# Performance work log

Measured on AMD Instinct MI355X. Metric: run time of the kernel, lower is better.

Reference implementation:

```python
import jax, jax.numpy as jnp
import numpy as np

NUM_HEADS = 12

def _get_rel_pos(q_size, k_size, rel_pos):
    # rel_pos already has shape (2*max(q,k)-1, head_dim) -> no resize needed
    q_coords = jnp.arange(q_size)[:, None] * max(k_size / q_size, 1.0)
    k_coords = jnp.arange(k_size)[None, :] * max(q_size / k_size, 1.0)
    rel = (q_coords - k_coords + (k_size - 1) * max(q_size / k_size, 1.0)).astype(jnp.int32)
    return rel_pos[rel.reshape(-1)].reshape(q_size, k_size, -1)  # (q, k, head_dim)


def setup_inputs() -> dict:
    key = jax.random.key(0)
    ks = jax.random.split(key, 7)
    B, H, W, C = 1, 64, 64, 768
    head_dim = C // NUM_HEADS
    return {
        "x": jax.random.normal(ks[0], (B, H, W, C), jnp.float32),
        "qkv_w": jax.random.normal(ks[1], (C, 3 * C), jnp.float32) * 0.02,
        "qkv_b": jax.random.normal(ks[2], (3 * C,), jnp.float32) * 0.02,
        "rel_pos_h": jax.random.normal(ks[3], (2 * H - 1, head_dim), jnp.float32) * 0.02,
        "rel_pos_w": jax.random.normal(ks[4], (2 * W - 1, head_dim), jnp.float32) * 0.02,
        "proj_w": jax.random.normal(ks[5], (C, C), jnp.float32) * 0.02,
        "proj_b": jax.random.normal(ks[6], (C,), jnp.float32) * 0.02,
    }


def reference(x, qkv_w, qkv_b, rel_pos_h, rel_pos_w, proj_w, proj_b):
    B, H, W, C = x.shape
    nh = NUM_HEADS
    hd = C // nh
    scale = hd ** (-0.5)
    S = H * W

    qkv = x @ qkv_w + qkv_b                              # (B,H,W,3C)
    qkv = qkv.reshape(B, S, 3, nh, hd).transpose(2, 0, 3, 1, 4).reshape(3, B * nh, S, hd)
    q, k, v = qkv[0], qkv[1], qkv[2]                     # (B*nh, S, hd)

    attn = jnp.einsum('bqd,bkd->bqk', q * scale, k)      # (B*nh, S, S)

    rh = _get_rel_pos(H, H, rel_pos_h)                   # (H,H,hd)
    rw = _get_rel_pos(W, W, rel_pos_w)                   # (W,W,hd)
    r_q = q.reshape(B * nh, H, W, hd)
    rel_h = jnp.einsum('bhwc,hkc->bhwk', r_q, rh)        # (B*nh,H,W,H)
    rel_w = jnp.einsum('bhwc,wkc->bhwk', r_q, rw)        # (B*nh,H,W,W)
    attn = (attn.reshape(B * nh, H, W, H, W)
            + rel_h[:, :, :, :, None]
            + rel_w[:, :, :, None, :]).reshape(B * nh, S, S)

    attn = jax.nn.softmax(attn, axis=-1)
    out = jnp.einsum('bqk,bkd->bqd', attn, v)            # (B*nh, S, hd)
    out = out.reshape(B, nh, H, W, hd).transpose(0, 2, 3, 1, 4).reshape(B, H, W, C)
    return out @ proj_w + proj_b
```

## Files before the change

### kernel.cpp

```cpp
#include <hip/hip_runtime.h>
#include <hip/hip_bf16.h>

#define S_TOK 4096
#define CDIM  768
#define N3C   2304
#define NH    12
#define HD    64

#define LOG2E 1.44269504f

typedef __attribute__((ext_vector_type(8))) short short8;
typedef __attribute__((ext_vector_type(4))) short short4v;
typedef __attribute__((ext_vector_type(4))) float float4v;
typedef __attribute__((ext_vector_type(4))) unsigned uint4v;

__device__ __forceinline__ float b2f(short s) {
    return __uint_as_float(((unsigned)(unsigned short)s) << 16);
}
__device__ __forceinline__ short f2b(float f) {
    unsigned u = __float_as_uint(f);
    unsigned r = (u + 0x7FFFu + ((u >> 16) & 1u)) >> 16;
    return (short)r;
}

#if __has_builtin(__builtin_amdgcn_exp2f)
#define EXP2F __builtin_amdgcn_exp2f
#else
#define EXP2F exp2f
#endif

__device__ __forceinline__ unsigned pack_trunc(float a, float b) {
    return __builtin_amdgcn_perm(__float_as_uint(b), __float_as_uint(a), 0x07060302u);
}

__device__ __forceinline__ short8 u4_to_s8(unsigned a, unsigned b, unsigned c, unsigned d) {
    union { uint4v u; short8 s; } t;
    t.u = (uint4v){a, b, c, d};
    return t.s;
}

__device__ __forceinline__ void load_lds16(const void* g, void* l) {
    __builtin_amdgcn_global_load_lds(
        (const __attribute__((address_space(1))) unsigned int*)g,
        (__attribute__((address_space(3))) unsigned int*)l, 16, 0, 0);
}

__global__ __launch_bounds__(256) void cast_bf16_kernel(
    const float* __restrict__ in, short* __restrict__ out, int n4)
{
    int i = blockIdx.x * 256 + threadIdx.x;
    if (i >= n4) return;
    float4 v = ((const float4*)in)[i];
    short4v o4 = { f2b(v.x), f2b(v.y), f2b(v.z), f2b(v.w) };
    *(short4v*)&out[(size_t)i * 4] = o4;
}

__global__ __launch_bounds__(256) void transpose_cast_kernel(
    const float* __restrict__ in, short* __restrict__ out, int R, int C)
{
    __shared__ float t[64][65];
    const int tid = threadIdx.x;
    const int c0 = blockIdx.x * 64, r0 = blockIdx.y * 64;
    const int li = tid >> 6;
    const int lj = tid & 63;
#pragma unroll
    for (int p = 0; p < 16; ++p) {
        int i = p * 4 + li;
        t[i][lj] = in[(size_t)(r0 + i) * C + c0 + lj];
    }
    __syncthreads();
#pragma unroll
    for (int p = 0; p < 16; ++p) {
        int i = p * 4 + li;
        out[(size_t)(c0 + i) * R + r0 + lj] = f2b(t[lj][i]);
    }
}

#define GEMM_CORE(A_, Bt_)                                                     \
    __shared__ __align__(16) short smem[2][128][64];                           \
    auto a_s = smem[0];                                                        \
    auto b_s = smem[1];                                                        \
    const int tid  = threadIdx.x;                                              \
    const int m0 = blockIdx.y * 128;                                           \
    const int n0 = blockIdx.x * 128;                                           \
    const int lane = tid & 63, w = tid >> 6;                                   \
    const int l15 = lane & 15, quad = lane >> 4;                               \
    const int wr = w >> 1, wc = w & 1;                                         \
    const int roff0 = (quad ^ (l15 & 7)) << 4;                                 \
    const int roff1 = roff0 ^ 64;                                              \
    const int srow0 = w * 8 + (lane >> 3);                                     \
    const int sslot = (lane & 7) ^ ((lane >> 3) & 7);                          \
    const short* ga = A_ + (size_t)(m0 + srow0) * 768 + sslot * 8;             \
    const short* gb = Bt_ + (size_t)(n0 + srow0) * 768 + sslot * 8;            \
    short* la = &a_s[w * 8][0];                                                \
    short* lb = &b_s[w * 8][0];                                                \
    float4v acc[4][4];                                                         \
    _Pragma("unroll")                                                          \
    for (int i = 0; i < 4; ++i)                                                \
        _Pragma("unroll")                                                      \
        for (int j = 0; j < 4; ++j) acc[i][j] = (float4v){0.f,0.f,0.f,0.f};    \
    for (int k0 = 0; k0 < 768; k0 += 64) {                                     \
        __syncthreads();                                                       \
        _Pragma("unroll")                                                      \
        for (int i = 0; i < 4; ++i) {                                          \
            load_lds16(ga + (size_t)i * (32 * 768) + k0, la + i * 32 * 64);    \
            load_lds16(gb + (size_t)i * (32 * 768) + k0, lb + i * 32 * 64);    \
        }                                                                      \
        __syncthreads();                                                       \
        _Pragma("unroll")                                                      \
        for (int kk = 0; kk < 64; kk += 32) {                                  \
            const int roff = kk ? roff1 : roff0;                               \
            short8 af[4], bfr[4];                                              \
            _Pragma("unroll")                                                  \
            for (int i = 0; i < 4; ++i)                                        \
                af[i] = *(const short8*)((const char*)&a_s[wr*64 + i*16 + l15][0] + roff); \
            _Pragma("unroll")                                                  \
            for (int j = 0; j < 4; ++j)                                        \
                bfr[j] = *(const short8*)((const char*)&b_s[wc*64 + j*16 + l15][0] + roff); \
            _Pragma("unroll")                                                  \
            for (int i = 0; i < 4; ++i)                                        \
                _Pragma("unroll")                                              \
                for (int j = 0; j < 4; ++j)                                    \
                    acc[i][j] = __builtin_amdgcn_mfma_f32_16x16x32_bf16(       \
                        af[i], bfr[j], acc[i][j], 0, 0, 0);                    \
        }                                                                      \
    }

__global__ __launch_bounds__(256) void gemm_qkv_mfma(
    const short* __restrict__ A, const short* __restrict__ Bt,
    const float* __restrict__ bias,
    short* __restrict__ Qb, short* __restrict__ Kb, short* __restrict__ Vt)
{
    GEMM_CORE(A, Bt)

    const int sec = n0 / CDIM;
    float bj[4];
#pragma unroll
    for (int j = 0; j < 4; ++j) bj[j] = bias[n0 + wc*64 + j*16 + l15];

    if (sec < 2) {
        short* base = (sec == 0) ? Qb : Kb;
        short (*tile)[68] = (short(*)[68])&smem[0][0][0];
#pragma unroll
        for (int h = 0; h < 2; ++h) {
            __syncthreads();
            if (wc == h) {
#pragma unroll
                for (int i = 0; i < 4; ++i)
#pragma unroll
                    for (int j = 0; j < 4; ++j)
#pragma unroll
                        for (int r = 0; r < 4; ++r)
                            tile[wr*64 + i*16 + quad*4 + r][j*16 + l15] =
                                f2b(acc[i][j][r] + bj[j]);
            }
            __syncthreads();
            const int nn = (n0 % CDIM) + h * 64;
            const int head = nn >> 6;
            short* dst = base + ((size_t)head * S_TOK + m0) * HD;
#pragma unroll
            for (int it = 0; it < 4; ++it) {
                const int row = it * 32 + (tid >> 3), c = (tid & 7) * 8;
                *(short8*)&dst[(size_t)row * HD + c] = *(const short8*)&tile[row][c];
            }
        }
    } else {
        short (*tv)[130] = (short(*)[130])&smem[0][0][0];
#pragma unroll
        for (int h = 0; h < 2; ++h) {
            __syncthreads();
            if (wc == h) {
#pragma unroll
                for (int i = 0; i < 4; ++i)
#pragma unroll
                    for (int j = 0; j < 4; ++j) {
                        short4v v4;
#pragma unroll
                        for (int r = 0; r < 4; ++r) v4[r] = f2b(acc[i][j][r] + bj[j]);
                        *(short4v*)&tv[j*16 + l15][wr*64 + i*16 + quad*4] = v4;
                    }
            }
            __syncthreads();
            const int nn = (n0 % CDIM) + h * 64;
            const int head = nn >> 6;
            short* dst = Vt + (size_t)head * HD * S_TOK + m0;
#pragma unroll
            for (int it = 0; it < 4; ++it) {
                const int nr = it * 16 + (tid >> 4), sc = (tid & 15) * 8;
                *(short8*)&dst[(size_t)nr * S_TOK + sc] = *(const short8*)&tv[nr][sc];
            }
        }
    }
}

__global__ __launch_bounds__(256) void gemm_proj_mfma(
    const short* __restrict__ A, const short* __restrict__ Bt,
    const float* __restrict__ bias, float* __restrict__ out)
{
    GEMM_CORE(A, Bt)

    float bj[4];
#pragma unroll
    for (int j = 0; j < 4; ++j) bj[j] = bias[n0 + wc*64 + j*16 + l15];

    float* tf = (float*)&smem[0][0][0];
#pragma unroll
    for (int h = 0; h < 2; ++h) {
        __syncthreads();
        if (wr == h) {
#pragma unroll
            for (int i = 0; i < 4; ++i)
#pragma unroll
                for (int j = 0; j < 4; ++j) {
                    const int cc = wc*16 + j*4 + (l15 >> 2);
                    const int ci = l15 & 3;
#pragma unroll
                    for (int r = 0; r < 4; ++r) {
                        const int row = i*16 + quad*4 + r;
                        const int pc = cc ^ ((row & 7) << 2);
                        tf[row * 128 + pc * 4 + ci] = acc[i][j][r] + bj[j];
                    }
                }
        }
        __syncthreads();
        float* dst = out + (size_t)(m0 + h * 64) * CDIM + n0;
#pragma unroll
        for (int it = 0; it < 8; ++it) {
            const int row = it * 8 + (tid >> 5);
            const int gc = tid & 31;
            const int pc = gc ^ ((row & 7) << 2);
            float4 v = *(const float4*)&tf[row * 128 + pc * 4];
            *(float4*)&dst[(size_t)row * CDIM + gc * 4] = v;
        }
    }
}

__global__ __launch_bounds__(256) void rel_mfma_kernel(
    const short* __restrict__ Qb, const float* __restrict__ rph,
    const float* __restrict__ rpw, short* __restrict__ RelhT,
    short* __restrict__ Relw)
{
    __shared__ __align__(16) short q_s [64][72];
    __shared__ __align__(16) short rh_s[64][72];
    __shared__ __align__(16) short rw_s[128][72];

    const int tid  = threadIdx.x;
    const int y    = blockIdx.x;
    const int head = blockIdx.y;
    const int s0   = y * 64;
    const int w = tid >> 6, lane = tid & 63;
    const int l15 = lane & 15, quad = lane >> 4;
    const int srow = tid >> 2;
    const int scol = (tid & 3) << 4;

    {
        const uint4* g = (const uint4*)(Qb + ((size_t)head * S_TOK + s0 + srow) * HD + scol);
        *(uint4*)&q_s[srow][scol]     = g[0];
        *(uint4*)&q_s[srow][scol + 8] = g[1];
    }
    {
        const float* g = rph + (size_t)(y + srow) * HD + scol;
        short tmp[16];
#pragma unroll
        for (int i = 0; i < 16; i += 4) {
            float4 v = *(const float4*)(g + i);
            tmp[i] = f2b(v.x); tmp[i+1] = f2b(v.y); tmp[i+2] = f2b(v.z); tmp[i+3] = f2b(v.w);
        }
        *(short8*)&rh_s[srow][scol]     = *(short8*)&tmp[0];
        *(short8*)&rh_s[srow][scol + 8] = *(short8*)&tmp[8];
    }
#pragma unroll
    for (int half = 0; half < 2; ++half) {
        const int row = srow + half * 64;
        const int rr  = row > 126 ? 126 : row;
        const float* g = rpw + (size_t)rr * HD + scol;
        short tmp[16];
#pragma unroll
        for (int i = 0; i < 16; i += 4) {
            float4 v = *(const float4*)(g + i);
            tmp[i] = f2b(v.x); tmp[i+1] = f2b(v.y); tmp[i+2] = f2b(v.z); tmp[i+3] = f2b(v.w);
        }
        *(short8*)&rw_s[row][scol]     = *(short8*)&tmp[0];
        *(short8*)&rw_s[row][scol + 8] = *(short8*)&tmp[8];
    }
    __syncthreads();

    const short8 qa0 = *(const short8*)&q_s[w * 16 + l15][quad * 8];
    const short8 qa1 = *(const short8*)&q_s[w * 16 + l15][32 + quad * 8];

#pragma unroll
    for (int ct = 0; ct < 4; ++ct) {
        const int jj = ct * 16 + l15;
        short8 b0 = *(const short8*)&rh_s[jj][quad * 8];
        short8 b1 = *(const short8*)&rh_s[jj][32 + quad * 8];
        float4v z = (float4v){0.f, 0.f, 0.f, 0.f};
        z = __builtin_amdgcn_mfma_f32_16x16x32_bf16(qa0, b0, z, 0, 0, 0);
        z = __builtin_amdgcn_mfma_f32_16x16x32_bf16(qa1, b1, z, 0, 0, 0);
        const int ky = 63 - jj;
        short4v o4;
#pragma unroll
        for (int r = 0; r < 4; ++r) o4[r] = f2b(z[r] * LOG2E);
        *(short4v*)&RelhT[((size_t)head * HD + ky) * S_TOK + s0 + w * 16 + quad * 4] = o4;
    }

#pragma unroll
    for (int ct = 0; ct < 8; ++ct) {
        const int j = ct * 16 + l15;
        short8 b0 = *(const short8*)&rw_s[j][quad * 8];
        short8 b1 = *(const short8*)&rw_s[j][32 + quad * 8];
        float4v z = (float4v){0.f, 0.f, 0.f, 0.f};
        z = __builtin_amdgcn_mfma_f32_16x16x32_bf16(qa0, b0, z, 0, 0, 0);
        z = __builtin_amdgcn_mfma_f32_16x16x32_bf16(qa1, b1, z, 0, 0, 0);
#pragma unroll
        for (int r = 0; r < 4; ++r) {
            const int q  = w * 16 + quad * 4 + r;
            const int kx = q + 63 - j;
            if (kx >= 0 && kx < 64)
                Relw[((size_t)head * S_TOK + s0 + q) * HD + kx] = f2b(z[r] * LOG2E);
        }
    }
}

__global__ __launch_bounds__(256, 3) void flash_kernel(
    const short* __restrict__ Qb, const short* __restrict__ Kb,
    const short* __restrict__ Vt, const short* __restrict__ RelhT,
    const short* __restrict__ Relw, short* __restrict__ attn_b)
{
    __shared__ __align__(16) short lds_s[24576];

    const int tid  = threadIdx.x;
    const int bid  = blockIdx.x;
    const int logi = (bid & 7) * 96 + (bid >> 3);
    const int head = logi >> 6;
    const int s0   = (logi & 63) << 6;
    const int w    = tid >> 6, lane = tid & 63;
    const int l15  = lane & 15, quad = lane >> 4;
    const int ph   = w >> 1;
    const int qh   = w & 1;

    const float C1 = 0.125f * LOG2E;

    const int lj = lane >> 3;
    const int sl = (lane & 7) ^ lj;
    const int kf0 = (lj & 3) + ((lj & 4) << 1) + qh * 32;

    const short* pKs = Kb + (size_t)head * S_TOK * HD
                     + (size_t)(ph * 32 * 64 + kf0) * HD + sl * 8;
    const short* pVs = Vt + ((size_t)head * HD + qh * 32 + lj) * S_TOK
                     + ph * 32 * 64 + sl * 8;

    short* lk0 = &lds_s[(ph * 2 + 0) << 12] + qh * 32 * 64;
    short* lk1 = &lds_s[(ph * 2 + 1) << 12] + qh * 32 * 64;
    short* lv  = &lds_s[16384 + (ph << 12)] + qh * 32 * 64;
    const short* krd0 = &lds_s[(ph * 2 + 0) << 12];
    const short* krd1 = &lds_s[(ph * 2 + 1) << 12];
    const short* vrd  = &lds_s[16384 + (ph << 12)];

    const int roff0 = (quad ^ (l15 & 7)) << 4;
    const int roff1 = roff0 ^ 64;

    short8 qb[2][2];
#pragma unroll
    for (int qt = 0; qt < 2; ++qt) {
        const short* qrow = Qb + ((size_t)head * S_TOK + s0 + qh * 32 + qt * 16 + l15) * HD;
        qb[qt][0] = *(const short8*)(qrow + quad * 8);
        qb[qt][1] = *(const short8*)(qrow + 32 + quad * 8);
    }

    float rwv[2][4][4];
#pragma unroll
    for (int qt = 0; qt < 2; ++qt) {
        const short* rwrow = Relw + ((size_t)head * S_TOK + s0 + qh * 32 + qt * 16 + l15) * HD;
#pragma unroll
        for (int kt = 0; kt < 4; ++kt) {
            const int base = ((kt & 1) << 2) | ((kt >> 1) << 5);
            short4v v = *(const short4v*)(rwrow + base + quad * 8);
#pragma unroll
            for (int r = 0; r < 4; ++r) rwv[qt][kt][r] = b2f(v[r]);
        }
    }

    const short* rhbase = RelhT + (size_t)head * HD * S_TOK + s0 + qh * 32 + l15;
    float rhc0 = b2f(rhbase[(size_t)(ph * 32) * S_TOK]);
    float rhc1 = b2f(rhbase[(size_t)(ph * 32) * S_TOK + 16]);

    short8 aones;
#pragma unroll
    for (int j = 0; j < 8; ++j) aones[j] = (short)0x3F80;

    float4v od[2][4];
#pragma unroll
    for (int qt = 0; qt < 2; ++qt)
#pragma unroll
        for (int dt = 0; dt < 4; ++dt) od[qt][dt] = (float4v){0.f, 0.f, 0.f, 0.f};
    float4v dq0 = (float4v){0.f, 0.f, 0.f, 0.f};
    float4v dq1 = (float4v){0.f, 0.f, 0.f, 0.f};

    load_lds16(pKs,        lk0);
    load_lds16(pKs + 1024, lk0 + 8  * 64);
    load_lds16(pKs + 256,  lk0 + 16 * 64);
    load_lds16(pKs + 1280, lk0 + 24 * 64);
    __syncthreads();

    for (int t = 0; t < 32; ++t) {
        const int cur = t & 1;
        const short* krd = cur ? krd1 : krd0;
        short* lkn = cur ? lk0 : lk1;

        load_lds16(pVs,               lv);
        load_lds16(pVs + 8  * S_TOK,  lv + 8  * 64);
        load_lds16(pVs + 16 * S_TOK,  lv + 16 * 64);
        load_lds16(pVs + 24 * S_TOK,  lv + 24 * 64);
        if (t < 31) {
            const short* pk = pKs + 4096;
            load_lds16(pk,        lkn);
            load_lds16(pk + 1024, lkn + 8  * 64);
            load_lds16(pk + 256,  lkn + 16 * 64);
            load_lds16(pk + 1280, lkn + 24 * 64);
        }
        pKs += 4096;
        pVs += 64;

        short rhn0, rhn1;
        if (t < 31) {
            rhn0 = rhbase[(size_t)(ph * 32 + t + 1) * S_TOK];
            rhn1 = rhbase[(size_t)(ph * 32 + t + 1) * S_TOK + 16];
        }

        unsigned pkk[2][8];
#pragma unroll
        for (int kt = 0; kt < 4; ++kt) {
            const char* krp = (const char*)(krd + (kt * 16 + l15) * 64);
            const short8 ka0 = *(const short8*)(krp + roff0);
            const short8 ka1 = *(const short8*)(krp + roff1);
            {
                float4v z = (float4v){0.f, 0.f, 0.f, 0.f};
                z = __builtin_amdgcn_mfma_f32_16x16x32_bf16(ka0, qb[0][0], z, 0, 0, 0);
                z = __builtin_amdgcn_mfma_f32_16x16x32_bf16(ka1, qb[0][1], z, 0, 0, 0);
                float p0 = EXP2F(C1 * z[0] + (rhc0 + rwv[0][kt][0]));
                float p1 = EXP2F(C1 * z[1] + (rhc0 + rwv[0][kt][1]));
                float p2 = EXP2F(C1 * z[2] + (rhc0 + rwv[0][kt][2]));
                float p3 = EXP2F(C1 * z[3] + (rhc0 + rwv[0][kt][3]));
                pkk[0][kt * 2]     = pack_trunc(p0, p1);
                pkk[0][kt * 2 + 1] = pack_trunc(p2, p3);
            }
            {
                float4v z = (float4v){0.f, 0.f, 0.f, 0.f};
                z = __builtin_amdgcn_mfma_f32_16x16x32_bf16(ka0, qb[1][0], z, 0, 0, 0);
                z = __builtin_amdgcn_mfma_f32_16x16x32_bf16(ka1, qb[1][1], z, 0, 0, 0);
                float p0 = EXP2F(C1 * z[0] + (rhc1 + rwv[1][kt][0]));
                float p1 = EXP2F(C1 * z[1] + (rhc1 + rwv[1][kt][1]));
                float p2 = EXP2F(C1 * z[2] + (rhc1 + rwv[1][kt][2]));
                float p3 = EXP2F(C1 * z[3] + (rhc1 + rwv[1][kt][3]));
                pkk[1][kt * 2]     = pack_trunc(p0, p1);
                pkk[1][kt * 2 + 1] = pack_trunc(p2, p3);
            }
        }
        const short8 pb00 = u4_to_s8(pkk[0][0], pkk[0][1], pkk[0][2], pkk[0][3]);
        const short8 pb01 = u4_to_s8(pkk[0][4], pkk[0][5], pkk[0][6], pkk[0][7]);
        const short8 pb10 = u4_to_s8(pkk[1][0], pkk[1][1], pkk[1][2], pkk[1][3]);
        const short8 pb11 = u4_to_s8(pkk[1][4], pkk[1][5], pkk[1][6], pkk[1][7]);

        __syncthreads();

        __builtin_amdgcn_s_setprio(1);
#pragma unroll
        for (int dt = 0; dt < 4; ++dt) {
            const char* vrp = (const char*)(vrd + (dt * 16 + l15) * 64);
            const short8 va0 = *(const short8*)(vrp + roff0);
            const short8 va1 = *(const short8*)(vrp + roff1);
            od[0][dt] = __builtin_amdgcn_mfma_f32_16x16x32_bf16(va0, pb00, od[0][dt], 0, 0, 0);
            od[0][dt] = __builtin_amdgcn_mfma_f32_16x16x32_bf16(va1, pb01, od[0][dt], 0, 0, 0);
            od[1][dt] = __builtin_amdgcn_mfma_f32_16x16x32_bf16(va0, pb10, od[1][dt], 0, 0, 0);
            od[1][dt] = __builtin_amdgcn_mfma_f32_16x16x32_bf16(va1, pb11, od[1][dt], 0, 0, 0);
        }
        dq0 = __builtin_amdgcn_mfma_f32_16x16x32_bf16(aones, pb00, dq0, 0, 0, 0);
        dq0 = __builtin_amdgcn_mfma_f32_16x16x32_bf16(aones, pb01, dq0, 0, 0, 0);
        dq1 = __builtin_amdgcn_mfma_f32_16x16x32_bf16(aones, pb10, dq1, 0, 0, 0);
        dq1 = __builtin_amdgcn_mfma_f32_16x16x32_bf16(aones, pb11, dq1, 0, 0, 0);
        __builtin_amdgcn_s_setprio(0);

        if (t < 31) {
            rhc0 = b2f(rhn0);
            rhc1 = b2f(rhn1);
        }
        __syncthreads();
    }

    float* cf = (float*)lds_s;
    if (ph == 1) {
#pragma unroll
        for (int qt = 0; qt < 2; ++qt)
#pragma unroll
            for (int dt = 0; dt < 4; ++dt) {
                float* dst = &cf[((((qh * 2 + qt) * 4 + dt) * 16) + quad * 4) * 16 + l15];
#pragma unroll
                for (int r = 0; r < 4; ++r) dst[r * 16] = od[qt][dt][r];
            }
        if (quad == 0) {
            cf[4096 + (qh * 2 + 0) * 16 + l15] = dq0[0];
            cf[4096 + (qh * 2 + 1) * 16 + l15] = dq1[0];
        }
    }
    __syncthreads();
    if (ph == 0) {
#pragma unroll
        for (int qt = 0; qt < 2; ++qt) {
            const float dtot = ((qt == 0) ? dq0[0] : dq1[0])
                             + cf[4096 + (qh * 2 + qt) * 16 + l15];
            const float inv = 1.f / dtot;
            short* outp = attn_b + (size_t)(s0 + qh * 32 + qt * 16 + l15) * CDIM + head * HD;
#pragma unroll
            for (int dt = 0; dt < 4; ++dt) {
                const float* src = &cf[((((qh * 2 + qt) * 4 + dt) * 16) + quad * 4) * 16 + l15];
                short4v o4;
#pragma unroll
                for (int r = 0; r < 4; ++r)
                    o4[r] = f2b((od[qt][dt][r] + src[r * 16]) * inv);
                *(short4v*)(outp + dt * 16 + quad * 4) = o4;
            }
        }
    }
}

extern "C" void kernel_launch(void* const* d_in, const int* in_sizes, int n_in,
                              void* d_out, int out_size, void* d_ws, size_t ws_size,
                              hipStream_t stream)
{
    const float* x    = (const float*)d_in[0];
    const float* qkvw = (const float*)d_in[1];
    const float* qkvb = (const float*)d_in[2];
    const float* rph  = (const float*)d_in[3];
    const float* rpw  = (const float*)d_in[4];
    const float* pw   = (const float*)d_in[5];
    const float* pb   = (const float*)d_in[6];
    float* out = (float*)d_out;

    const size_t HSD = (size_t)NH * S_TOK * HD;
    short* xb     = (short*)d_ws;
    short* wt     = xb + (size_t)S_TOK * CDIM;
    short* pwt    = wt + (size_t)N3C * CDIM;
    short* Qb     = pwt + (size_t)CDIM * CDIM;
    short* Kb     = Qb + HSD;
    short* Vt     = Kb + HSD;
    short* RelhT  = Vt + HSD;
    short* Relw   = RelhT + HSD;
    short* attn_b = Relw + HSD;

    cast_bf16_kernel<<<S_TOK * CDIM / 4 / 256, 256, 0, stream>>>(x, xb, S_TOK * CDIM / 4);
    transpose_cast_kernel<<<dim3(N3C / 64, CDIM / 64), 256, 0, stream>>>(qkvw, wt, CDIM, N3C);
    transpose_cast_kernel<<<dim3(CDIM / 64, CDIM / 64), 256, 0, stream>>>(pw, pwt, CDIM, CDIM);

    gemm_qkv_mfma<<<dim3(N3C / 128, S_TOK / 128), 256, 0, stream>>>(
        xb, wt, qkvb, Qb, Kb, Vt);
    rel_mfma_kernel<<<dim3(64, NH), 256, 0, stream>>>(Qb, rph, rpw, RelhT, Relw);
    flash_kernel<<<dim3(64 * NH), 256, 0, stream>>>(Qb, Kb, Vt, RelhT, Relw, attn_b);
    gemm_proj_mfma<<<dim3(CDIM / 128, S_TOK / 128), 256, 0, stream>>>(
        attn_b, pwt, pb, out);
}
```

Before: 210.6 us.

## Use partial vmcnt waits and raw barriers to overlap K/V loads with compute

Replaces the full __syncthreads in the attention main loop with explicit s_waitcnt vmcnt(N) counts plus s_barrier. Each phase now waits only for the loads it needs (K before the score phase, V before the PV phase), so the next tile's K prefetch stays in flight during compute. The last iteration is peeled out so the loop body has no t<31 branches. This relies on the exact in-flight load counts matching the compiler's instruction order; a wrong count would cause a race on LDS.

```diff
diff --git a/kernel.cpp b/kernel.cpp
--- a/kernel.cpp
+++ b/kernel.cpp
@@ -402,7 +402,60 @@
     load_lds16(pKs + 1280, lk0 + 24 * 64);
     __syncthreads();
 
-    for (int t = 0; t < 32; ++t) {
+#define S_PHASE(krd_)                                                          \
+        unsigned pkk[2][8];                                                    \
+        _Pragma("unroll")                                                      \
+        for (int kt = 0; kt < 4; ++kt) {                                       \
+            const char* krp = (const char*)((krd_) + (kt * 16 + l15) * 64);    \
+            const short8 ka0 = *(const short8*)(krp + roff0);                  \
+            const short8 ka1 = *(const short8*)(krp + roff1);                  \
+            {                                                                  \
+                float4v z = (float4v){0.f, 0.f, 0.f, 0.f};                     \
+                z = __builtin_amdgcn_mfma_f32_16x16x32_bf16(ka0, qb[0][0], z, 0, 0, 0); \
+                z = __builtin_amdgcn_mfma_f32_16x16x32_bf16(ka1, qb[0][1], z, 0, 0, 0); \
+                float p0 = EXP2F(C1 * z[0] + (rhc0 + rwv[0][kt][0]));          \
+                float p1 = EXP2F(C1 * z[1] + (rhc0 + rwv[0][kt][1]));          \
+                float p2 = EXP2F(C1 * z[2] + (rhc0 + rwv[0][kt][2]));          \
+                float p3 = EXP2F(C1 * z[3] + (rhc0 + rwv[0][kt][3]));          \
+                pkk[0][kt * 2]     = pack_trunc(p0, p1);                       \
+                pkk[0][kt * 2 + 1] = pack_trunc(p2, p3);                       \
+            }                                                                  \
+            {                                                                  \
+                float4v z = (float4v){0.f, 0.f, 0.f, 0.f};                     \
+                z = __builtin_amdgcn_mfma_f32_16x16x32_bf16(ka0, qb[1][0], z, 0, 0, 0); \
+                z = __builtin_amdgcn_mfma_f32_16x16x32_bf16(ka1, qb[1][1], z, 0, 0, 0); \
+                float p0 = EXP2F(C1 * z[0] + (rhc1 + rwv[1][kt][0]));          \
+                float p1 = EXP2F(C1 * z[1] + (rhc1 + rwv[1][kt][1]));          \
+                float p2 = EXP2F(C1 * z[2] + (rhc1 + rwv[1][kt][2]));          \
+                float p3 = EXP2F(C1 * z[3] + (rhc1 + rwv[1][kt][3]));          \
+                pkk[1][kt * 2]     = pack_trunc(p0, p1);                       \
+                pkk[1][kt * 2 + 1] = pack_trunc(p2, p3);                       \
+            }                                                                  \
+        }                                                                      \
+        const short8 pb00 = u4_to_s8(pkk[0][0], pkk[0][1], pkk[0][2], pkk[0][3]); \
+        const short8 pb01 = u4_to_s8(pkk[0][4], pkk[0][5], pkk[0][6], pkk[0][7]); \
+        const short8 pb10 = u4_to_s8(pkk[1][0], pkk[1][1], pkk[1][2], pkk[1][3]); \
+        const short8 pb11 = u4_to_s8(pkk[1][4], pkk[1][5], pkk[1][6], pkk[1][7]);
+
+#define PV_PHASE                                                               \
+        __builtin_amdgcn_s_setprio(1);                                         \
+        _Pragma("unroll")                                                      \
+        for (int dt = 0; dt < 4; ++dt) {                                       \
+            const char* vrp = (const char*)(vrd + (dt * 16 + l15) * 64);       \
+            const short8 va0 = *(const short8*)(vrp + roff0);                  \
+            const short8 va1 = *(const short8*)(vrp + roff1);                  \
+            od[0][dt] = __builtin_amdgcn_mfma_f32_16x16x32_bf16(va0, pb00, od[0][dt], 0, 0, 0); \
+            od[0][dt] = __builtin_amdgcn_mfma_f32_16x16x32_bf16(va1, pb01, od[0][dt], 0, 0, 0); \
+            od[1][dt] = __builtin_amdgcn_mfma_f32_16x16x32_bf16(va0, pb10, od[1][dt], 0, 0, 0); \
+            od[1][dt] = __builtin_amdgcn_mfma_f32_16x16x32_bf16(va1, pb11, od[1][dt], 0, 0, 0); \
+        }                                                                      \
+        dq0 = __builtin_amdgcn_mfma_f32_16x16x32_bf16(aones, pb00, dq0, 0, 0, 0); \
+        dq0 = __builtin_amdgcn_mfma_f32_16x16x32_bf16(aones, pb01, dq0, 0, 0, 0); \
+        dq1 = __builtin_amdgcn_mfma_f32_16x16x32_bf16(aones, pb10, dq1, 0, 0, 0); \
+        dq1 = __builtin_amdgcn_mfma_f32_16x16x32_bf16(aones, pb11, dq1, 0, 0, 0); \
+        __builtin_amdgcn_s_setprio(0);
+
+    for (int t = 0; t < 31; ++t) {
         const int cur = t & 1;
         const short* krd = cur ? krd1 : krd0;
         short* lkn = cur ? lk0 : lk1;
@@ -411,7 +464,11 @@
         load_lds16(pVs + 8  * S_TOK,  lv + 8  * 64);
         load_lds16(pVs + 16 * S_TOK,  lv + 16 * 64);
         load_lds16(pVs + 24 * S_TOK,  lv + 24 * 64);
-        if (t < 31) {
+        asm volatile("" ::: "memory");
+        short rhn0 = rhbase[(size_t)(ph * 32 + t + 1) * S_TOK];
+        short rhn1 = rhbase[(size_t)(ph * 32 + t + 1) * S_TOK + 16];
+        asm volatile("" ::: "memory");
+        {
             const short* pk = pKs + 4096;
             load_lds16(pk,        lkn);
             load_lds16(pk + 1024, lkn + 8  * 64);
@@ -421,71 +478,45 @@
         pKs += 4096;
         pVs += 64;
 
-        short rhn0, rhn1;
-        if (t < 31) {
-            rhn0 = rhbase[(size_t)(ph * 32 + t + 1) * S_TOK];
-            rhn1 = rhbase[(size_t)(ph * 32 + t + 1) * S_TOK + 16];
-        }
-
-        unsigned pkk[2][8];
-#pragma unroll
-        for (int kt = 0; kt < 4; ++kt) {
-            const char* krp = (const char*)(krd + (kt * 16 + l15) * 64);
-            const short8 ka0 = *(const short8*)(krp + roff0);
-            const short8 ka1 = *(const short8*)(krp + roff1);
-            {
-                float4v z = (float4v){0.f, 0.f, 0.f, 0.f};
-                z = __builtin_amdgcn_mfma_f32_16x16x32_bf16(ka0, qb[0][0], z, 0, 0, 0);
-                z = __builtin_amdgcn_mfma_f32_16x16x32_bf16(ka1, qb[0][1], z, 0, 0, 0);
-                float p0 = EXP2F(C1 * z[0] + (rhc0 + rwv[0][kt][0]));
-                float p1 = EXP2F(C1 * z[1] + (rhc0 + rwv[0][kt][1]));
-                float p2 = EXP2F(C1 * z[2] + (rhc0 + rwv[0][kt][2]));
-                float p3 = EXP2F(C1 * z[3] + (rhc0 + rwv[0][kt][3]));
-                pkk[0][kt * 2]     = pack_trunc(p0, p1);
-                pkk[0][kt * 2 + 1] = pack_trunc(p2, p3);
-            }
-            {
-                float4v z = (float4v){0.f, 0.f, 0.f, 0.f};
-                z = __builtin_amdgcn_mfma_f32_16x16x32_bf16(ka0, qb[1][0], z, 0, 0, 0);
-                z = __builtin_amdgcn_mfma_f32_16x16x32_bf16(ka1, qb[1][1], z, 0, 0, 0);
-                float p0 = EXP2F(C1 * z[0] + (rhc1 + rwv[1][kt][0]));
-                float p1 = EXP2F(C1 * z[1] + (rhc1 + rwv[1][kt][1]));
-                float p2 = EXP2F(C1 * z[2] + (rhc1 + rwv[1][kt][2]));
-                float p3 = EXP2F(C1 * z[3] + (rhc1 + rwv[1][kt][3]));
-                pkk[1][kt * 2]     = pack_trunc(p0, p1);
-                pkk[1][kt * 2 + 1] = pack_trunc(p2, p3);
-            }
-        }
-        const short8 pb00 = u4_to_s8(pkk[0][0], pkk[0][1], pkk[0][2], pkk[0][3]);
-        const short8 pb01 = u4_to_s8(pkk[0][4], pkk[0][5], pkk[0][6], pkk[0][7]);
-        const short8 pb10 = u4_to_s8(pkk[1][0], pkk[1][1], pkk[1][2], pkk[1][3]);
-        const short8 pb11 = u4_to_s8(pkk[1][4], pkk[1][5], pkk[1][6], pkk[1][7]);
-
-        __syncthreads();
-
-        __builtin_amdgcn_s_setprio(1);
-#pragma unroll
-        for (int dt = 0; dt < 4; ++dt) {
-            const char* vrp = (const char*)(vrd + (dt * 16 + l15) * 64);
-            const short8 va0 = *(const short8*)(vrp + roff0);
-            const short8 va1 = *(const short8*)(vrp + roff1);
-            od[0][dt] = __builtin_amdgcn_mfma_f32_16x16x32_bf16(va0, pb00, od[0][dt], 0, 0, 0);
-            od[0][dt] = __builtin_amdgcn_mfma_f32_16x16x32_bf16(va1, pb01, od[0][dt], 0, 0, 0);
-            od[1][dt] = __builtin_amdgcn_mfma_f32_16x16x32_bf16(va0, pb10, od[1][dt], 0, 0, 0);
-            od[1][dt] = __builtin_amdgcn_mfma_f32_16x16x32_bf16(va1, pb11, od[1][dt], 0, 0, 0);
-        }
-        dq0 = __builtin_amdgcn_mfma_f32_16x16x32_bf16(aones, pb00, dq0, 0, 0, 0);
-        dq0 = __builtin_amdgcn_mfma_f32_16x16x32_bf16(aones, pb01, dq0, 0, 0, 0);
-        dq1 = __builtin_amdgcn_mfma_f32_16x16x32_bf16(aones, pb10, dq1, 0, 0, 0);
-        dq1 = __builtin_amdgcn_mfma_f32_16x16x32_bf16(aones, pb11, dq1, 0, 0, 0);
-        __builtin_amdgcn_s_setprio(0);
-
-        if (t < 31) {
-            rhc0 = b2f(rhn0);
-            rhc1 = b2f(rhn1);
-        }
-        __syncthreads();
-    }
+        asm volatile("s_waitcnt vmcnt(10)" ::: "memory");
+        __builtin_amdgcn_sched_barrier(0);
+        __builtin_amdgcn_s_barrier();
+
+        S_PHASE(krd)
+
+        asm volatile("s_waitcnt vmcnt(6)" ::: "memory");
+        __builtin_amdgcn_sched_barrier(0);
+        __builtin_amdgcn_s_barrier();
+
+        PV_PHASE
+
+        rhc0 = b2f(rhn0);
+        rhc1 = b2f(rhn1);
+
+        __builtin_amdgcn_s_barrier();
+    }
+
+    {
+        const short* krd = krd1;
+        load_lds16(pVs,               lv);
+        load_lds16(pVs + 8  * S_TOK,  lv + 8  * 64);
+        load_lds16(pVs + 16 * S_TOK,  lv + 16 * 64);
+        load_lds16(pVs + 24 * S_TOK,  lv + 24 * 64);
+
+        asm volatile("s_waitcnt vmcnt(4)" ::: "memory");
+        __builtin_amdgcn_sched_barrier(0);
+        __builtin_amdgcn_s_barrier();
+
+        S_PHASE(krd)
+
+        asm volatile("s_waitcnt vmcnt(0)" ::: "memory");
+        __builtin_amdgcn_sched_barrier(0);
+        __builtin_amdgcn_s_barrier();
+
+        PV_PHASE
+    }
+#undef S_PHASE
+#undef PV_PHASE
 
     float* cf = (float*)lds_s;
     if (ph == 1) {
```

After: 210.3 us. Within noise of the previous version (-0.2%).
